# Kernel tuning notes

Measured on AMD Instinct MI355X. Metric: run time of the kernel, lower is better.

Reference implementation:

```python
import jax, jax.numpy as jnp
import numpy as np

CH = 8        # MASK_HEAD.CHANNELS
CIN = 8       # MASK_BRANCH.OUT_CHANNELS
# weight/bias split offsets for 3-layer head with rel coords:
# w0=(CIN+2)*CH=80, w1=CH*CH=64, w2=CH*1=8, b0=8, b1=8, b2=1 -> 169


def _bilinear_align_corners(x, Ho, Wo):
    # x: [n, c, H, W] -> [n, c, Ho, Wo], matches F.interpolate(align_corners=True)
    n, c, H, W = x.shape
    ys = jnp.arange(Ho, dtype=x.dtype) * ((H - 1) / (Ho - 1))
    xs = jnp.arange(Wo, dtype=x.dtype) * ((W - 1) / (Wo - 1))
    y0 = jnp.floor(ys).astype(jnp.int32)
    y1 = jnp.minimum(y0 + 1, H - 1)
    wy = (ys - y0.astype(x.dtype))[:, None]
    x0 = jnp.floor(xs).astype(jnp.int32)
    x1 = jnp.minimum(x0 + 1, W - 1)
    wx = xs - x0.astype(x.dtype)
    rows = x[..., y0, :] * (1.0 - wy) + x[..., y1, :] * wy   # [n,c,Ho,W]
    out = rows[..., x0] * (1.0 - wx) + rows[..., x1] * wx    # [n,c,Ho,Wo]
    return out


def setup_inputs() -> dict:
    key = jax.random.key(0)
    k1, k2, k3, k4, k5, k6 = jax.random.split(key, 6)
    N, H, W = 2, 128, 192
    n_inst = 256
    stride = 8
    mask_feats = jax.random.normal(k1, (N, CIN, H, W), dtype=jnp.float32)
    mask_head_params = jax.random.normal(k2, (n_inst, 169), dtype=jnp.float32) * 0.1
    # instance center locations in image coords (stride-8 feature covers [0, W*stride))
    instance_locations = jax.random.uniform(k3, (n_inst, 2), dtype=jnp.float32) * jnp.array(
        [W * stride, H * stride], dtype=jnp.float32
    )
    fpn_levels = jax.random.randint(k4, (n_inst,), 0, 5, dtype=jnp.int32)
    soi_table = jnp.array([64.0, 128.0, 256.0, 512.0, 1024.0], dtype=jnp.float32)
    sizes_of_interest = soi_table[fpn_levels]  # pre-gathered soi per instance
    im_inds = jax.random.randint(k5, (n_inst,), 0, N, dtype=jnp.int32)
    return {
        "mask_feats": mask_feats,
        "mask_head_params": mask_head_params,
        "instance_locations": instance_locations,
        "sizes_of_interest": sizes_of_interest,
        "im_inds": im_inds,
        "fpn_levels": fpn_levels,
        "mask_feat_stride": 8,
    }


def reference(mask_feats, mask_head_params, instance_locations, sizes_of_interest,
              im_inds, fpn_levels, mask_feat_stride):
    N, _, H, W = mask_feats.shape
    n_inst = mask_head_params.shape[0]
    dt = mask_feats.dtype

    # compute_locations(H, W, stride): (x, y) centers of the mask-feat grid
    shifts_x = jnp.arange(W, dtype=dt) * mask_feat_stride + mask_feat_stride // 2
    shifts_y = jnp.arange(H, dtype=dt) * mask_feat_stride + mask_feat_stride // 2
    xx, yy = jnp.meshgrid(shifts_x, shifts_y)              # [H, W]
    locations = jnp.stack([xx.ravel(), yy.ravel()], axis=1)  # [HW, 2]

    # relative coords per instance, normalized by size-of-interest of its FPN level
    rel = instance_locations[:, None, :] - locations[None, :, :]   # [n, HW, 2]
    rel = jnp.transpose(rel, (0, 2, 1)) / sizes_of_interest[:, None, None]  # [n, 2, HW]

    feats = mask_feats[im_inds].reshape(n_inst, CIN, H * W)        # gather per instance
    x = jnp.concatenate([rel.astype(dt), feats], axis=1).reshape(n_inst, CIN + 2, H, W)

    p = mask_head_params
    w0 = p[:, 0:80].reshape(n_inst, CH, CIN + 2)
    w1 = p[:, 80:144].reshape(n_inst, CH, CH)
    w2 = p[:, 144:152].reshape(n_inst, 1, CH)
    b0 = p[:, 152:160]
    b1 = p[:, 160:168]
    b2 = p[:, 168:169]

    # per-instance 1x1 convs == batched small GEMMs over the spatial grid
    x = jax.nn.relu(jnp.einsum('noc,nchw->nohw', w0, x) + b0[:, :, None, None])
    x = jax.nn.relu(jnp.einsum('noc,nchw->nohw', w1, x) + b1[:, :, None, None])
    x = jnp.einsum('noc,nchw->nohw', w2, x) + b2[:, :, None, None]  # [n,1,H,W]

    # inference path: F.interpolate(scale_factor=2, mode='bilinear', align_corners=True)
    return _bilinear_align_corners(x, 2 * H, 2 * W)
```

## Files before the change

### kernel.cpp

```cpp
#include <hip/hip_runtime.h>

typedef float f32x4 __attribute__((ext_vector_type(4)));

#define HH 128
#define WW 192
#define HO 256
#define WO 384
#define NINST 256
#define OTY 64
#define LTYMAX 34
#define LPAD 196
#define STRIPS 24

__global__ __launch_bounds__(256) void dynmask_fused(
    const float* __restrict__ feats,
    const float* __restrict__ params,
    const float* __restrict__ locs,
    const float* __restrict__ soi,
    const int*   __restrict__ im_inds,
    const int*   __restrict__ stride_p,
    float* __restrict__ out)
{
    const int n   = blockIdx.y;
    const int t   = threadIdx.x;
    const int oy0 = blockIdx.x * OTY;

    __shared__ float tile[LTYMAX][LPAD];

    const float sy = 127.0f / 255.0f;
    const float sx = 191.0f / 383.0f;

    const int ly0    = (int)((float)oy0 * sy);
    int lylast       = (int)((float)(oy0 + OTY - 1) * sy) + 1;
    if (lylast > HH - 1) lylast = HH - 1;
    const int lcount = lylast - ly0 + 1;

    const float* __restrict__ pw = params + n * 169;
    const int   stride  = *stride_p;
    const float inv_soi = 1.0f / soi[n];
    const float loc_x   = locs[2*n+0];
    const float loc_y   = locs[2*n+1];
    const float* fbase  = feats + im_inds[n] * (8*HH*WW);

    const float xstep = -(float)stride * inv_soi;

    const int nstrips = lcount * STRIPS;
    for (int s = t; s < nstrips; s += 256) {
        const int r  = s / STRIPS;
        const int c0 = (s - r*STRIPS) * 8;
        const int gy = ly0 + r;
        const float* frow = fbase + gy*WW + c0;

        const float yrel = (loc_y - (float)(gy*stride + (stride>>1))) * inv_soi;
        const float xr0  = (loc_x - (float)(c0*stride + (stride>>1))) * inv_soi;

        #pragma unroll
        for (int g = 0; g < 2; ++g) {
            f32x4 f[8];
            #pragma unroll
            for (int ch = 0; ch < 8; ++ch)
                f[ch] = *(const f32x4*)(frow + ch*(HH*WW) + g*4);

            float xr[4];
            #pragma unroll
            for (int j = 0; j < 4; ++j)
                xr[j] = fmaf((float)(g*4+j), xstep, xr0);

            float h0[4][8];
            #pragma unroll
            for (int o = 0; o < 8; ++o) {
                const float wxw = pw[o*10+0];
                const float wyw = pw[o*10+1];
                const float b0w = pw[152+o];
                #pragma unroll
                for (int j = 0; j < 4; ++j) {
                    float a = fmaf(xr[j], wxw, fmaf(yrel, wyw, b0w));
                    #pragma unroll
                    for (int ch = 0; ch < 8; ++ch)
                        a = fmaf(f[ch][j], pw[o*10+2+ch], a);
                    h0[j][o] = fmaxf(a, 0.0f);
                }
            }

            float res[4];
            #pragma unroll
            for (int j = 0; j < 4; ++j) res[j] = pw[168];
            #pragma unroll
            for (int o = 0; o < 8; ++o) {
                const float b1w = pw[160+o];
                const float w2w = pw[144+o];
                #pragma unroll
                for (int j = 0; j < 4; ++j) {
                    float a = b1w;
                    #pragma unroll
                    for (int c = 0; c < 8; ++c)
                        a = fmaf(h0[j][c], pw[80+o*8+c], a);
                    res[j] = fmaf(fmaxf(a, 0.0f), w2w, res[j]);
                }
            }

            f32x4 rv; rv[0]=res[0]; rv[1]=res[1]; rv[2]=res[2]; rv[3]=res[3];
            *(f32x4*)&tile[r][c0 + g*4] = rv;
        }
    }

    __syncthreads();

    float* obase = out + (size_t)n * (HO*WO);
    #pragma unroll
    for (int k = 0; k < 24; ++k) {
        const int v   = t + k*256;
        const int row = (int)((unsigned)v / 96u);
        const int xv  = v - row*96;
        const int yo  = oy0 + row;

        const float ysf = (float)yo * sy;
        int iy0 = (int)ysf; if (iy0 > HH-2) iy0 = HH-2;
        const float wy = ysf - (float)iy0;
        const float* r0 = tile[iy0 - ly0];
        const float* r1 = tile[iy0 - ly0 + 1];

        float* orow = obase + yo*WO + xv;
        #pragma unroll
        for (int j = 0; j < 4; ++j) {
            const int xo = xv + 96*j;
            const float xsf = (float)xo * sx;
            int ix0 = (int)xsf; if (ix0 > WW-2) ix0 = WW-2;
            const float wxf = xsf - (float)ix0;
            float a = r0[ix0], b = r0[ix0+1];
            float c = r1[ix0], d = r1[ix0+1];
            float va = fmaf(wy, c - a, a);
            float vb = fmaf(wy, d - b, b);
            orow[96*j] = fmaf(wxf, vb - va, va);
        }
    }
}

extern "C" void kernel_launch(void* const* d_in, const int* in_sizes, int n_in,
                              void* d_out, int out_size, void* d_ws, size_t ws_size,
                              hipStream_t stream) {
    const float* feats    = (const float*)d_in[0];
    const float* params   = (const float*)d_in[1];
    const float* locs     = (const float*)d_in[2];
    const float* soi      = (const float*)d_in[3];
    const int*   im_inds  = (const int*)d_in[4];
    const int*   stride_p = (const int*)d_in[6];
    float* out = (float*)d_out;

    dim3 grid(HO / OTY, NINST);
    dim3 block(256);
    hipLaunchKernelGGL(dynmask_fused, grid, block, 0, stream,
                       feats, params, locs, soi, im_inds, stride_p, out);
}
```

Baseline: 56.59 us.

## Use packed FP32 FMAs for the MLP and one output column per thread

Rewrites the per-pixel 3-layer MLP on 2-wide float vectors so the compiler can emit packed FP32 FMA/max instructions, roughly halving the instruction count of the compute phase. The block grows from 256 to 384 threads so that each thread owns one output column (WO=384) in the upsample phase. Each thread then walks 64 rows, with the horizontal interpolation index and weight computed once per column instead of per output pixel. The larger block may reduce occupancy and changes how the strips are spread across threads.

```diff
diff --git a/kernel.cpp b/kernel.cpp
--- a/kernel.cpp
+++ b/kernel.cpp
@@ -1,5 +1,6 @@
 #include <hip/hip_runtime.h>
 
+typedef float f32x2 __attribute__((ext_vector_type(2)));
 typedef float f32x4 __attribute__((ext_vector_type(4)));
 
 #define HH 128
@@ -11,8 +12,27 @@
 #define LTYMAX 34
 #define LPAD 196
 #define STRIPS 24
+#define NT 384
 
-__global__ __launch_bounds__(256) void dynmask_fused(
+static __device__ __forceinline__ f32x2 splat2(float v) { f32x2 r; r.x = v; r.y = v; return r; }
+
+static __device__ __forceinline__ f32x2 pkfma(f32x2 a, float w, f32x2 c) {
+#if __has_builtin(__builtin_elementwise_fma)
+    return __builtin_elementwise_fma(a, splat2(w), c);
+#else
+    f32x2 r; r.x = fmaf(a.x, w, c.x); r.y = fmaf(a.y, w, c.y); return r;
+#endif
+}
+
+static __device__ __forceinline__ f32x2 relu2(f32x2 a) {
+#if __has_builtin(__builtin_elementwise_max)
+    return __builtin_elementwise_max(a, splat2(0.0f));
+#else
+    f32x2 r; r.x = fmaxf(a.x, 0.0f); r.y = fmaxf(a.y, 0.0f); return r;
+#endif
+}
+
+__global__ __launch_bounds__(NT) void dynmask_fused(
     const float* __restrict__ feats,
     const float* __restrict__ params,
     const float* __restrict__ locs,
@@ -45,7 +65,7 @@
     const float xstep = -(float)stride * inv_soi;
 
     const int nstrips = lcount * STRIPS;
-    for (int s = t; s < nstrips; s += 256) {
+    for (int s = t; s < nstrips; s += NT) {
         const int r  = s / STRIPS;
         const int c0 = (s - r*STRIPS) * 8;
         const int gy = ly0 + r;
@@ -61,78 +81,72 @@
             for (int ch = 0; ch < 8; ++ch)
                 f[ch] = *(const f32x4*)(frow + ch*(HH*WW) + g*4);
 
-            float xr[4];
-            #pragma unroll
-            for (int j = 0; j < 4; ++j)
-                xr[j] = fmaf((float)(g*4+j), xstep, xr0);
+            f32x2 xp0, xp1;
+            xp0.x = fmaf((float)(g*4+0), xstep, xr0);
+            xp0.y = fmaf((float)(g*4+1), xstep, xr0);
+            xp1.x = fmaf((float)(g*4+2), xstep, xr0);
+            xp1.y = fmaf((float)(g*4+3), xstep, xr0);
 
-            float h0[4][8];
+            f32x2 h0a[8], h0b[8];
             #pragma unroll
             for (int o = 0; o < 8; ++o) {
+                const float byo = fmaf(yrel, pw[o*10+1], pw[152+o]);
                 const float wxw = pw[o*10+0];
-                const float wyw = pw[o*10+1];
-                const float b0w = pw[152+o];
+                f32x2 a0 = pkfma(xp0, wxw, splat2(byo));
+                f32x2 a1 = pkfma(xp1, wxw, splat2(byo));
                 #pragma unroll
-                for (int j = 0; j < 4; ++j) {
-                    float a = fmaf(xr[j], wxw, fmaf(yrel, wyw, b0w));
-                    #pragma unroll
-                    for (int ch = 0; ch < 8; ++ch)
-                        a = fmaf(f[ch][j], pw[o*10+2+ch], a);
-                    h0[j][o] = fmaxf(a, 0.0f);
+                for (int ch = 0; ch < 8; ++ch) {
+                    const float w = pw[o*10+2+ch];
+                    a0 = pkfma(f[ch].xy, w, a0);
+                    a1 = pkfma(f[ch].zw, w, a1);
                 }
+                h0a[o] = relu2(a0);
+                h0b[o] = relu2(a1);
             }
 
-            float res[4];
-            #pragma unroll
-            for (int j = 0; j < 4; ++j) res[j] = pw[168];
+            f32x2 res0 = splat2(pw[168]);
+            f32x2 res1 = splat2(pw[168]);
             #pragma unroll
             for (int o = 0; o < 8; ++o) {
                 const float b1w = pw[160+o];
                 const float w2w = pw[144+o];
+                f32x2 a0 = splat2(b1w);
+                f32x2 a1 = splat2(b1w);
                 #pragma unroll
-                for (int j = 0; j < 4; ++j) {
-                    float a = b1w;
-                    #pragma unroll
-                    for (int c = 0; c < 8; ++c)
-                        a = fmaf(h0[j][c], pw[80+o*8+c], a);
-                    res[j] = fmaf(fmaxf(a, 0.0f), w2w, res[j]);
+                for (int c = 0; c < 8; ++c) {
+                    const float w = pw[80+o*8+c];
+                    a0 = pkfma(h0a[c], w, a0);
+                    a1 = pkfma(h0b[c], w, a1);
                 }
+                res0 = pkfma(relu2(a0), w2w, res0);
+                res1 = pkfma(relu2(a1), w2w, res1);
             }
 
-            f32x4 rv; rv[0]=res[0]; rv[1]=res[1]; rv[2]=res[2]; rv[3]=res[3];
+            f32x4 rv; rv.x = res0.x; rv.y = res0.y; rv.z = res1.x; rv.w = res1.y;
             *(f32x4*)&tile[r][c0 + g*4] = rv;
         }
     }
 
     __syncthreads();
 
-    float* obase = out + (size_t)n * (HO*WO);
-    #pragma unroll
-    for (int k = 0; k < 24; ++k) {
-        const int v   = t + k*256;
-        const int row = (int)((unsigned)v / 96u);
-        const int xv  = v - row*96;
-        const int yo  = oy0 + row;
+    const float xsf = (float)t * sx;
+    int ix0 = (int)xsf; if (ix0 > WW-2) ix0 = WW-2;
+    const float wxf = xsf - (float)ix0;
 
+    float* ocol = out + (size_t)n * (HO*WO) + (size_t)oy0 * WO + t;
+    #pragma unroll 4
+    for (int row = 0; row < OTY; ++row) {
+        const int   yo  = oy0 + row;
         const float ysf = (float)yo * sy;
         int iy0 = (int)ysf; if (iy0 > HH-2) iy0 = HH-2;
         const float wy = ysf - (float)iy0;
-        const float* r0 = tile[iy0 - ly0];
-        const float* r1 = tile[iy0 - ly0 + 1];
-
-        float* orow = obase + yo*WO + xv;
-        #pragma unroll
-        for (int j = 0; j < 4; ++j) {
-            const int xo = xv + 96*j;
-            const float xsf = (float)xo * sx;
-            int ix0 = (int)xsf; if (ix0 > WW-2) ix0 = WW-2;
-            const float wxf = xsf - (float)ix0;
-            float a = r0[ix0], b = r0[ix0+1];
-            float c = r1[ix0], d = r1[ix0+1];
-            float va = fmaf(wy, c - a, a);
-            float vb = fmaf(wy, d - b, b);
-            orow[96*j] = fmaf(wxf, vb - va, va);
-        }
+        const float* r0 = &tile[iy0 - ly0][0] + ix0;
+        const float* r1 = r0 + LPAD;
+        float a = r0[0], b = r0[1];
+        float c = r1[0], d = r1[1];
+        float va = fmaf(wy, c - a, a);
+        float vb = fmaf(wy, d - b, b);
+        ocol[row * WO] = fmaf(wxf, vb - va, va);
     }
 }
 
@@ -148,7 +162,7 @@
     float* out = (float*)d_out;
 
     dim3 grid(HO / OTY, NINST);
-    dim3 block(256);
+    dim3 block(NT);
     hipLaunchKernelGGL(dynmask_fused, grid, block, 0, stream,
                        feats, params, locs, soi, im_inds, stride_p, out);
 }
```

Result: slower. 121.0 us (+113.9%).

## Split output into 32-row pairs and overlap MLP with upsampling stages

Applied to the files above, without the earlier changes.

Each block now covers 32 output rows instead of 64, giving 2048 blocks over a 1D grid with instance-major indexing. Within a block it computes the MLP for the first 10 low-res rows, upsamples the first 16 output rows, then computes the next 8 low-res rows and upsamples the second half. The aim is to overlap compute with stores and shrink shared memory per block. The upsample loop walks columns down rows and reuses the previous row's taps to cut LDS reads. The cost is an extra barrier and more blocks recomputing the overlapping boundary rows.

```diff
diff --git a/kernel.cpp b/kernel.cpp
--- a/kernel.cpp
+++ b/kernel.cpp
@@ -7,12 +7,118 @@
 #define HO 256
 #define WO 384
 #define NINST 256
-#define OTY 64
-#define LTYMAX 34
+#define NPX (HH*WW)
 #define LPAD 196
-#define STRIPS 24
+#define SPAN 18
 
-__global__ __launch_bounds__(256) void dynmask_fused(
+__device__ __forceinline__ void mlp_strip(
+    const float* __restrict__ frow,
+    const float* __restrict__ pw,
+    float yrel, float xr0, float xstep,
+    float* __restrict__ dst)
+{
+    float byo[8];
+    #pragma unroll
+    for (int o = 0; o < 8; ++o)
+        byo[o] = fmaf(yrel, pw[o*10+1], pw[152+o]);
+
+    #pragma unroll
+    for (int g = 0; g < 2; ++g) {
+        f32x4 f[8];
+        #pragma unroll
+        for (int ch = 0; ch < 8; ++ch)
+            f[ch] = *(const f32x4*)(frow + ch*NPX + g*4);
+
+        float xr[4];
+        #pragma unroll
+        for (int j = 0; j < 4; ++j)
+            xr[j] = fmaf((float)(g*4+j), xstep, xr0);
+
+        float h0[4][8];
+        #pragma unroll
+        for (int o = 0; o < 8; ++o) {
+            const float wxw = pw[o*10+0];
+            #pragma unroll
+            for (int j = 0; j < 4; ++j) {
+                float a = fmaf(xr[j], wxw, byo[o]);
+                #pragma unroll
+                for (int ch = 0; ch < 8; ++ch)
+                    a = fmaf(f[ch][j], pw[o*10+2+ch], a);
+                h0[j][o] = fmaxf(a, 0.0f);
+            }
+        }
+
+        f32x4 rv;
+        #pragma unroll
+        for (int j = 0; j < 4; ++j) rv[j] = pw[168];
+        #pragma unroll
+        for (int o = 0; o < 8; ++o) {
+            const float b1w = pw[160+o];
+            const float w2w = pw[144+o];
+            #pragma unroll
+            for (int j = 0; j < 4; ++j) {
+                float a = b1w;
+                #pragma unroll
+                for (int c = 0; c < 8; ++c)
+                    a = fmaf(h0[j][c], pw[80+o*8+c], a);
+                rv[j] = fmaf(fmaxf(a, 0.0f), w2w, rv[j]);
+            }
+        }
+        *(f32x4*)(dst + g*4) = rv;
+    }
+}
+
+__device__ __forceinline__ void upsample_band(
+    const float* __restrict__ tile0,
+    int ly00, int oy0, int t,
+    float* __restrict__ obase)
+{
+    const float sy = 127.0f / 255.0f;
+    const float sx = 191.0f / 383.0f;
+
+    #pragma unroll
+    for (int k = 0; k < 3; ++k) {
+        const int u    = t + k*256;
+        const int wrap = (u >= 384);
+        const int col  = wrap ? u - 384 : u;
+        const int r0o  = wrap ? 8 : 0;
+
+        const float xsf = (float)col * sx;
+        int ix0 = (int)xsf; if (ix0 > WW-2) ix0 = WW-2;
+        const float wx = xsf - (float)ix0;
+        const float* tcol = tile0 + ix0;
+
+        float a, b, c, d;
+        int prevIy = -999;
+        float* optr = obase + (size_t)(oy0 + r0o) * WO + col;
+
+        for (int rr = 0; rr < 8; ++rr) {
+            const int   yo  = oy0 + r0o + rr;
+            const float ysf = (float)yo * sy;
+            int iy0 = (int)ysf; if (iy0 > HH-2) iy0 = HH-2;
+            const float wy = ysf - (float)iy0;
+
+            if (iy0 != prevIy) {
+                const float* p = tcol + (iy0 - ly00) * LPAD;
+                if (iy0 == prevIy + 1) {
+                    a = c; b = d;
+                    c = p[LPAD]; d = p[LPAD+1];
+                } else {
+                    a = p[0];    b = p[1];
+                    c = p[LPAD]; d = p[LPAD+1];
+                }
+                prevIy = iy0;
+            }
+
+            float va = fmaf(wy, c - a, a);
+            float vb = fmaf(wy, d - b, b);
+            *optr = fmaf(wx, vb - va, va);
+            optr += WO;
+        }
+    }
+}
+
+__global__ __launch_bounds__(256) void dynmask_pipe(
     const float* __restrict__ feats,
     const float* __restrict__ params,
     const float* __restrict__ locs,
@@ -21,119 +127,51 @@
     const int*   __restrict__ stride_p,
     float* __restrict__ out)
 {
-    const int n   = blockIdx.y;
-    const int t   = threadIdx.x;
-    const int oy0 = blockIdx.x * OTY;
+    const int b    = blockIdx.x;
+    const int n    = b & (NINST - 1);
+    const int pair = b >> 8;
+    const int t    = threadIdx.x;
+    const int oy0_0 = pair * 32;
+    const int oy0_1 = oy0_0 + 16;
 
-    __shared__ float tile[LTYMAX][LPAD];
+    __shared__ float tile[SPAN][LPAD];
 
     const float sy = 127.0f / 255.0f;
-    const float sx = 191.0f / 383.0f;
-
-    const int ly0    = (int)((float)oy0 * sy);
-    int lylast       = (int)((float)(oy0 + OTY - 1) * sy) + 1;
-    if (lylast > HH - 1) lylast = HH - 1;
-    const int lcount = lylast - ly0 + 1;
+    const int ly00 = (int)((float)oy0_0 * sy);
 
     const float* __restrict__ pw = params + n * 169;
     const int   stride  = *stride_p;
     const float inv_soi = 1.0f / soi[n];
     const float loc_x   = locs[2*n+0];
     const float loc_y   = locs[2*n+1];
-    const float* fbase  = feats + im_inds[n] * (8*HH*WW);
+    const float* fbase  = feats + im_inds[n] * (8*NPX);
+    const float xstep   = -(float)stride * inv_soi;
+    float* obase = out + (size_t)n * (HO*WO);
 
-    const float xstep = -(float)stride * inv_soi;
-
-    const int nstrips = lcount * STRIPS;
-    for (int s = t; s < nstrips; s += 256) {
-        const int r  = s / STRIPS;
-        const int c0 = (s - r*STRIPS) * 8;
-        const int gy = ly0 + r;
-        const float* frow = fbase + gy*WW + c0;
-
+    if (t < 240) {
+        const int r  = (unsigned)t / 24;
+        const int c0 = (t - r*24) * 8;
+        const int gy = ly00 + r;
         const float yrel = (loc_y - (float)(gy*stride + (stride>>1))) * inv_soi;
         const float xr0  = (loc_x - (float)(c0*stride + (stride>>1))) * inv_soi;
-
-        #pragma unroll
-        for (int g = 0; g < 2; ++g) {
-            f32x4 f[8];
-            #pragma unroll
-            for (int ch = 0; ch < 8; ++ch)
-                f[ch] = *(const f32x4*)(frow + ch*(HH*WW) + g*4);
-
-            float xr[4];
-            #pragma unroll
-            for (int j = 0; j < 4; ++j)
-                xr[j] = fmaf((float)(g*4+j), xstep, xr0);
-
-            float h0[4][8];
-            #pragma unroll
-            for (int o = 0; o < 8; ++o) {
-                const float wxw = pw[o*10+0];
-                const float wyw = pw[o*10+1];
-                const float b0w = pw[152+o];
-                #pragma unroll
-                for (int j = 0; j < 4; ++j) {
-                    float a = fmaf(xr[j], wxw, fmaf(yrel, wyw, b0w));
-                    #pragma unroll
-                    for (int ch = 0; ch < 8; ++ch)
-                        a = fmaf(f[ch][j], pw[o*10+2+ch], a);
-                    h0[j][o] = fmaxf(a, 0.0f);
-                }
-            }
-
-            float res[4];
-            #pragma unroll
-            for (int j = 0; j < 4; ++j) res[j] = pw[168];
-            #pragma unroll
-            for (int o = 0; o < 8; ++o) {
-                const float b1w = pw[160+o];
-                const float w2w = pw[144+o];
-                #pragma unroll
-                for (int j = 0; j < 4; ++j) {
-                    float a = b1w;
-                    #pragma unroll
-                    for (int c = 0; c < 8; ++c)
-                        a = fmaf(h0[j][c], pw[80+o*8+c], a);
-                    res[j] = fmaf(fmaxf(a, 0.0f), w2w, res[j]);
-                }
-            }
-
-            f32x4 rv; rv[0]=res[0]; rv[1]=res[1]; rv[2]=res[2]; rv[3]=res[3];
-            *(f32x4*)&tile[r][c0 + g*4] = rv;
-        }
+        mlp_strip(fbase + gy*WW + c0, pw, yrel, xr0, xstep, &tile[r][c0]);
     }
-
     __syncthreads();
 
-    float* obase = out + (size_t)n * (HO*WO);
-    #pragma unroll
-    for (int k = 0; k < 24; ++k) {
-        const int v   = t + k*256;
-        const int row = (int)((unsigned)v / 96u);
-        const int xv  = v - row*96;
-        const int yo  = oy0 + row;
+    upsample_band(&tile[0][0], ly00, oy0_0, t, obase);
 
-        const float ysf = (float)yo * sy;
-        int iy0 = (int)ysf; if (iy0 > HH-2) iy0 = HH-2;
-        const float wy = ysf - (float)iy0;
-        const float* r0 = tile[iy0 - ly0];
-        const float* r1 = tile[iy0 - ly0 + 1];
+    if (t < 192) {
+        const int rq = (unsigned)t / 24;
+        const int r  = 10 + rq;
+        const int c0 = (t - rq*24) * 8;
+        int gy = ly00 + r; if (gy > HH-1) gy = HH-1;
+        const float yrel = (loc_y - (float)(gy*stride + (stride>>1))) * inv_soi;
+        const float xr0  = (loc_x - (float)(c0*stride + (stride>>1))) * inv_soi;
+        mlp_strip(fbase + gy*WW + c0, pw, yrel, xr0, xstep, &tile[r][c0]);
+    }
+    __syncthreads();
 
-        float* orow = obase + yo*WO + xv;
-        #pragma unroll
-        for (int j = 0; j < 4; ++j) {
-            const int xo = xv + 96*j;
-            const float xsf = (float)xo * sx;
-            int ix0 = (int)xsf; if (ix0 > WW-2) ix0 = WW-2;
-            const float wxf = xsf - (float)ix0;
-            float a = r0[ix0], b = r0[ix0+1];
-            float c = r1[ix0], d = r1[ix0+1];
-            float va = fmaf(wy, c - a, a);
-            float vb = fmaf(wy, d - b, b);
-            orow[96*j] = fmaf(wxf, vb - va, va);
-        }
-    }
+    upsample_band(&tile[0][0], ly00, oy0_1, t, obase);
 }
 
 extern "C" void kernel_launch(void* const* d_in, const int* in_sizes, int n_in,
@@ -147,8 +185,6 @@
     const int*   stride_p = (const int*)d_in[6];
     float* out = (float*)d_out;
 
-    dim3 grid(HO / OTY, NINST);
-    dim3 block(256);
-    hipLaunchKernelGGL(dynmask_fused, grid, block, 0, stream,
+    hipLaunchKernelGGL(dynmask_pipe, dim3(2048), dim3(256), 0, stream,
                        feats, params, locs, soi, im_inds, stride_p, out);
 }
```

After: 55.24 us. 1.02x faster.

## Shrink output row tile to 16 and reuse column weights across rows in upsample

Applied to the files above, without the earlier changes.

Cuts the output tile from 64 to 16 rows per block. That gives four times as many blocks, and each thread computes at most one strip of the MLP, which removes the strip loop and the halo overcompute share shifts. The upsample pass now gives each thread one output column across eight rows. It computes the x-interpolation index and weight once and keeps the needed source rows in registers, using a hardcoded mapping from row to source row. This relies on exact knowledge of the scale factor and adds more halo recomputation per output row than the larger tile did.

```diff
diff --git a/kernel.cpp b/kernel.cpp
--- a/kernel.cpp
+++ b/kernel.cpp
@@ -7,10 +7,13 @@
 #define HO 256
 #define WO 384
 #define NINST 256
-#define OTY 64
-#define LTYMAX 34
+#define NPX (HH*WW)
+#define OTY 16
+#define LTY 10
 #define LPAD 196
 #define STRIPS 24
+#define SY (127.0f/255.0f)
+#define SX (191.0f/383.0f)
 
 __global__ __launch_bounds__(256) void dynmask_fused(
     const float* __restrict__ feats,
@@ -25,30 +28,22 @@
     const int t   = threadIdx.x;
     const int oy0 = blockIdx.x * OTY;
 
-    __shared__ float tile[LTYMAX][LPAD];
+    __shared__ float tile[LTY][LPAD];
 
-    const float sy = 127.0f / 255.0f;
-    const float sx = 191.0f / 383.0f;
-
-    const int ly0    = (int)((float)oy0 * sy);
-    int lylast       = (int)((float)(oy0 + OTY - 1) * sy) + 1;
-    if (lylast > HH - 1) lylast = HH - 1;
-    const int lcount = lylast - ly0 + 1;
+    const int ly0 = (int)((float)oy0 * SY);
 
     const float* __restrict__ pw = params + n * 169;
     const int   stride  = *stride_p;
     const float inv_soi = 1.0f / soi[n];
     const float loc_x   = locs[2*n+0];
     const float loc_y   = locs[2*n+1];
-    const float* fbase  = feats + im_inds[n] * (8*HH*WW);
+    const float* fbase  = feats + im_inds[n] * (8*NPX);
+    const float xstep   = -(float)stride * inv_soi;
 
-    const float xstep = -(float)stride * inv_soi;
-
-    const int nstrips = lcount * STRIPS;
-    for (int s = t; s < nstrips; s += 256) {
-        const int r  = s / STRIPS;
-        const int c0 = (s - r*STRIPS) * 8;
-        const int gy = ly0 + r;
+    if (t < LTY * STRIPS) {
+        const int r  = (unsigned)t / STRIPS;
+        const int c0 = (t - r*STRIPS) * 8;
+        int gy = ly0 + r; if (gy > HH-1) gy = HH-1;
         const float* frow = fbase + gy*WW + c0;
 
         const float yrel = (loc_y - (float)(gy*stride + (stride>>1))) * inv_soi;
@@ -59,7 +54,7 @@
             f32x4 f[8];
             #pragma unroll
             for (int ch = 0; ch < 8; ++ch)
-                f[ch] = *(const f32x4*)(frow + ch*(HH*WW) + g*4);
+                f[ch] = *(const f32x4*)(frow + ch*NPX + g*4);
 
             float xr[4];
             #pragma unroll
@@ -69,12 +64,11 @@
             float h0[4][8];
             #pragma unroll
             for (int o = 0; o < 8; ++o) {
+                const float byo = fmaf(yrel, pw[o*10+1], pw[152+o]);
                 const float wxw = pw[o*10+0];
-                const float wyw = pw[o*10+1];
-                const float b0w = pw[152+o];
                 #pragma unroll
                 for (int j = 0; j < 4; ++j) {
-                    float a = fmaf(xr[j], wxw, fmaf(yrel, wyw, b0w));
+                    float a = fmaf(xr[j], wxw, byo);
                     #pragma unroll
                     for (int ch = 0; ch < 8; ++ch)
                         a = fmaf(f[ch][j], pw[o*10+2+ch], a);
@@ -82,9 +76,9 @@
                 }
             }
 
-            float res[4];
+            f32x4 rv;
             #pragma unroll
-            for (int j = 0; j < 4; ++j) res[j] = pw[168];
+            for (int j = 0; j < 4; ++j) rv[j] = pw[168];
             #pragma unroll
             for (int o = 0; o < 8; ++o) {
                 const float b1w = pw[160+o];
@@ -95,11 +89,9 @@
                     #pragma unroll
                     for (int c = 0; c < 8; ++c)
                         a = fmaf(h0[j][c], pw[80+o*8+c], a);
-                    res[j] = fmaf(fmaxf(a, 0.0f), w2w, res[j]);
+                    rv[j] = fmaf(fmaxf(a, 0.0f), w2w, rv[j]);
                 }
             }
-
-            f32x4 rv; rv[0]=res[0]; rv[1]=res[1]; rv[2]=res[2]; rv[3]=res[3];
             *(f32x4*)&tile[r][c0 + g*4] = rv;
         }
     }
@@ -108,31 +100,69 @@
 
     float* obase = out + (size_t)n * (HO*WO);
     #pragma unroll
-    for (int k = 0; k < 24; ++k) {
-        const int v   = t + k*256;
-        const int row = (int)((unsigned)v / 96u);
-        const int xv  = v - row*96;
-        const int yo  = oy0 + row;
+    for (int k = 0; k < 3; ++k) {
+        const int u    = t + k*256;
+        const int wrap = (u >= 384);
+        const int col  = wrap ? u - 384 : u;
+        const int r0o  = wrap ? 8 : 0;
+        const int v0   = oy0 + r0o;
 
-        const float ysf = (float)yo * sy;
-        int iy0 = (int)ysf; if (iy0 > HH-2) iy0 = HH-2;
-        const float wy = ysf - (float)iy0;
-        const float* r0 = tile[iy0 - ly0];
-        const float* r1 = tile[iy0 - ly0 + 1];
+        const float xsf = (float)col * SX;
+        int ix0 = (int)xsf; if (ix0 > WW-2) ix0 = WW-2;
+        const float wx = xsf - (float)ix0;
 
-        float* orow = obase + yo*WO + xv;
-        #pragma unroll
-        for (int j = 0; j < 4; ++j) {
-            const int xo = xv + 96*j;
-            const float xsf = (float)xo * sx;
-            int ix0 = (int)xsf; if (ix0 > WW-2) ix0 = WW-2;
-            const float wxf = xsf - (float)ix0;
-            float a = r0[ix0], b = r0[ix0+1];
-            float c = r1[ix0], d = r1[ix0+1];
-            float va = fmaf(wy, c - a, a);
-            float vb = fmaf(wy, d - b, b);
-            orow[96*j] = fmaf(wxf, vb - va, va);
+        const float ysf0 = (float)v0 * SY;
+        const int   iyA  = (int)ysf0;
+        const int   base = iyA - ly0;
+        const float f0   = ysf0 - (float)iyA;
+
+        const float* tc = &tile[base][ix0];
+        float pa0 = tc[0],        pb0 = tc[1];
+        float pa1 = tc[1*LPAD],   pb1 = tc[1*LPAD+1];
+        float pa2 = tc[2*LPAD],   pb2 = tc[2*LPAD+1];
+        float pa3 = tc[3*LPAD],   pb3 = tc[3*LPAD+1];
+        float pa4 = tc[4*LPAD],   pb4 = tc[4*LPAD+1];
+        float pa5 = tc[5*LPAD],   pb5 = tc[5*LPAD+1];
+
+        float* optr = obase + (size_t)v0 * WO + col;
+
+        #define EMIT_ROW(RR, MLO)                                            \
+        {                                                                    \
+            const float wy = fmaf((float)(RR), SY, f0) - (float)(MLO);       \
+            const float va = fmaf(wy, pa##MLO##N - pa##MLO, pa##MLO);        \
+            const float vb = fmaf(wy, pb##MLO##N - pb##MLO, pb##MLO);        \
+            *optr = fmaf(wx, vb - va, va);                                   \
+            optr += WO;                                                      \
         }
+        #define pa0N pa1
+        #define pa1N pa2
+        #define pa2N pa3
+        #define pa3N pa4
+        #define pa4N pa5
+        #define pb0N pb1
+        #define pb1N pb2
+        #define pb2N pb3
+        #define pb3N pb4
+        #define pb4N pb5
+
+        if (v0 == 0) {
+            EMIT_ROW(0,0) EMIT_ROW(1,0) EMIT_ROW(2,0) EMIT_ROW(3,1)
+            EMIT_ROW(4,1) EMIT_ROW(5,2) EMIT_ROW(6,2) EMIT_ROW(7,3)
+        } else {
+            EMIT_ROW(0,0) EMIT_ROW(1,1) EMIT_ROW(2,1) EMIT_ROW(3,2)
+            EMIT_ROW(4,2) EMIT_ROW(5,3) EMIT_ROW(6,3) EMIT_ROW(7,4)
+        }
+        #undef EMIT_ROW
+        #undef pa0N
+        #undef pa1N
+        #undef pa2N
+        #undef pa3N
+        #undef pa4N
+        #undef pb0N
+        #undef pb1N
+        #undef pb2N
+        #undef pb3N
+        #undef pb4N
     }
 }
 
```

New measurement: 51.65 us. 8.7% less time.
